# Optimization experiments

Measured on AMD Instinct MI355X. Metric: run time of the kernel, lower is better.

The kernel has to match this reference:

```python
import jax, jax.numpy as jnp
import numpy as np

T = 5          # temporal frames
WS = 8         # window size (square)
HEADS = 6
DIM = 192      # output channels; qkv input channels = 3*DIM
SHIFT = WS // 2
HDIM = DIM // HEADS
SCALE = HDIM ** -0.5
N = T * WS * WS  # tokens per window = 320


def _rel_index():
    # Faithful replication of the torch buffer construction (including the
    # quirk that the dw channel gets no offset).
    coords = np.stack(np.meshgrid(np.arange(T), np.arange(WS), np.arange(WS), indexing='ij'))
    cf = coords.reshape(3, -1)                      # (3, N)
    rel = (cf[:, :, None] - cf[:, None, :]).transpose(1, 2, 0).astype(np.int64)
    rel[:, :, 0] += WS - 1                          # dt channel
    rel[:, :, 1] += WS - 1                          # dh channel
    rel[:, :, 0] *= 2 * WS - 1
    return rel.sum(-1)                               # (N, N) int

REL_INDEX = jnp.asarray(_rel_index())


def setup_inputs() -> dict:
    key = jax.random.key(0)
    k1, k2, k3, k4 = jax.random.split(key, 4)
    B, H, W = 2, 64, 64
    C = 3 * DIM
    qkv = jax.random.normal(k1, (B, T * H * W, C), jnp.float32)
    bias_table = jax.random.normal(k2, ((T * 2 * WS - 1) * (2 * WS - 1), HEADS), jnp.float32) * 0.02
    proj_w = jax.random.normal(k3, (DIM, DIM), jnp.float32) / np.sqrt(DIM)
    proj_b = jax.random.normal(k4, (DIM,), jnp.float32) * 0.01
    # Standard Swin shifted-window attention mask, tiled over T (t-outer order).
    img = np.zeros((H, W), np.float32)
    cnt = 0
    sls = (slice(0, -WS), slice(-WS, -SHIFT), slice(-SHIFT, None))
    for hs in sls:
        for ws_ in sls:
            img[hs, ws_] = cnt
            cnt += 1
    mw = img.reshape(H // WS, WS, W // WS, WS).transpose(0, 2, 1, 3).reshape(-1, WS * WS)
    mw = np.tile(mw, (1, T))                         # (nW, N)
    am = mw[:, None, :] - mw[:, :, None]
    mask = jnp.asarray(np.where(am != 0, -100.0, 0.0).astype(np.float32))
    return {'qkv': qkv, 'bias_table': bias_table, 'proj_w': proj_w,
            'proj_b': proj_b, 'mask': mask, 'H': H, 'W': W}


def reference(qkv, bias_table, proj_w, proj_b, mask, H, W):
    B, L, C = qkv.shape
    x = qkv.reshape(B, T, H, W, C)
    # cyclic shift
    x = jnp.roll(x, shift=(-SHIFT, -SHIFT), axis=(2, 3))
    # window partition -> (B*nW, N, C)
    x = x.reshape(B, T, H // WS, WS, W // WS, WS, C)
    x = x.transpose(0, 2, 4, 1, 3, 5, 6).reshape(-1, N, C)
    B_ = x.shape[0]
    qkv_ = x.reshape(B_, N, 3, HEADS, HDIM).transpose(2, 0, 3, 1, 4)  # (3,B_,h,N,d)
    q, k, v = qkv_[0] * SCALE, qkv_[1], qkv_[2]
    attn = jnp.einsum('bhqd,bhkd->bhqk', q, k)       # (B_, h, N, N)
    rpb = bias_table[REL_INDEX.reshape(-1)].reshape(N, N, HEADS).transpose(2, 0, 1)
    attn = attn + rpb[None]
    nW = mask.shape[0]
    attn = attn.reshape(B_ // nW, nW, HEADS, N, N) + mask[None, :, None]
    attn = jax.nn.softmax(attn.reshape(B_, HEADS, N, N), axis=-1)
    out = jnp.einsum('bhqk,bhkd->bhqd', attn, v)     # (B_, h, N, d)
    out = out.transpose(0, 2, 1, 3).reshape(B_, N, DIM)
    out = out @ proj_w.T + proj_b
    # window reverse -> (B, T, H, W, DIM)
    out = out.reshape(B, H // WS, W // WS, T, WS, WS, DIM)
    out = out.transpose(0, 3, 1, 4, 2, 5, 6).reshape(B, T, H, W, DIM)
    out = jnp.roll(out, shift=(SHIFT, SHIFT), axis=(2, 3))
    return out.reshape(B, T * H * W, DIM)
```

## Files before the change

### kernel.cpp

```cpp
#include <hip/hip_runtime.h>
#include <hip/hip_bf16.h>

#define TT      5
#define NHEADS  6
#define DIMC    192
#define SHIFT_  4
#define HDIM_   32
#define NTOK    320
#define NWIN    64
#define BATCH   2
#define LOG2E   1.44269504088896f
#define SCALE_LOG2E (0.17677669529663687f * 1.44269504088896f)
#define NEGMASK (-100.0f * 1.44269504088896f)

typedef short short8v __attribute__((ext_vector_type(8)));
typedef float floatx4 __attribute__((ext_vector_type(4)));
union FragU { uint4 u; short8v s; };

static __device__ __forceinline__ float bf16lo(unsigned u) {
    union { unsigned i; float f; } x; x.i = u << 16; return x.f;
}
static __device__ __forceinline__ float bf16hi(unsigned u) {
    union { unsigned i; float f; } x; x.i = u & 0xffff0000u; return x.f;
}
static __device__ __forceinline__ unsigned short bf16b(float f) {
    __hip_bfloat16 h = __float2bfloat16(f);
    unsigned short u; __builtin_memcpy(&u, &h, 2); return u;
}
static __device__ __forceinline__ unsigned pk2(float a, float b) {
    return (unsigned)bf16b(a) | ((unsigned)bf16b(b) << 16);
}

static __device__ __forceinline__ bool detect_bf16(const unsigned* q) {
    uint4 w = ((const uint4*)q)[threadIdx.x & 63];
    int cnt = 0;
    unsigned e;
    e = (w.x >> 7) & 0xffu; cnt += (e >= 100u && e <= 135u);
    e = (w.y >> 7) & 0xffu; cnt += (e >= 100u && e <= 135u);
    e = (w.z >> 7) & 0xffu; cnt += (e >= 100u && e <= 135u);
    e = (w.w >> 7) & 0xffu; cnt += (e >= 100u && e <= 135u);
    unsigned long long m = __ballot(cnt >= 2);
    return __popcll(m) >= 32;
}

__global__ __launch_bounds__(NTOK) void attn_mfma(
    const void* __restrict__ qkv_raw,
    const void* __restrict__ bias_raw,
    __hip_bfloat16* __restrict__ win_out)
{
    const bool isbf = detect_bf16((const unsigned*)qkv_raw);
    const int b_  = blockIdx.x;
    const int h   = blockIdx.y;
    const int bb  = b_ >> 6;
    const int wdx = b_ & 63;
    const int wi  = wdx >> 3, wj = wdx & 7;
    const int tid = threadIdx.x;
    const int w    = tid >> 6;
    const int lane = tid & 63;
    const int l15  = lane & 15;
    const int quad = lane >> 4;

    __shared__ unsigned short sK[320 * 40];
    __shared__ unsigned short sVT[32 * 328];
    __shared__ unsigned short sP[5 * 64 * 40];
    __shared__ float sRS[5 * 64];
    __shared__ float sBias[192];

    {
        const int n = tid;
        const int t = n >> 6, s = n & 63, hl = s >> 3, wl = s & 7;
        const int gh = (wi * 8 + hl + SHIFT_) & 63;
        const int gw = (wj * 8 + wl + SHIFT_) & 63;
        const long grow = (long)bb * (TT * 64 * 64) + t * 4096 + gh * 64 + gw;
        if (!isbf) {
            const float* base = (const float*)qkv_raw + grow * (3 * DIMC);
            const float* kp = base + DIMC + h * HDIM_;
            uint4* dst = (uint4*)&sK[n * 40];
            #pragma unroll
            for (int i = 0; i < 4; i++)
                dst[i] = make_uint4(pk2(kp[8*i+0], kp[8*i+1]), pk2(kp[8*i+2], kp[8*i+3]),
                                    pk2(kp[8*i+4], kp[8*i+5]), pk2(kp[8*i+6], kp[8*i+7]));
            const float* vp = base + 2 * DIMC + h * HDIM_;
            #pragma unroll
            for (int d = 0; d < 32; d++) sVT[d * 328 + n] = bf16b(vp[d]);
            for (int i = tid; i < 192; i += NTOK)
                sBias[i] = ((const float*)bias_raw)[i * NHEADS + h] * LOG2E;
        } else {
            const __hip_bfloat16* base = (const __hip_bfloat16*)qkv_raw + grow * (3 * DIMC);
            const uint4* kp = (const uint4*)(base + DIMC + h * HDIM_);
            uint4* dst = (uint4*)&sK[n * 40];
            #pragma unroll
            for (int i = 0; i < 4; i++) dst[i] = kp[i];
            const unsigned* vp = (const unsigned*)(base + 2 * DIMC + h * HDIM_);
            #pragma unroll
            for (int i = 0; i < 16; i++) {
                unsigned u = vp[i];
                sVT[(2*i+0) * 328 + n] = (unsigned short)(u & 0xffffu);
                sVT[(2*i+1) * 328 + n] = (unsigned short)(u >> 16);
            }
            for (int i = tid; i < 192; i += NTOK)
                sBias[i] = __bfloat162float(((const __hip_bfloat16*)bias_raw)[i * NHEADS + h]) * LOG2E;
        }
    }

    FragU qf[4];
    int cn_q[4], labq[4];
    #pragma unroll
    for (int jq = 0; jq < 4; jq++) {
        const int qtok = w * 64 + jq * 16 + l15;
        const int t = qtok >> 6, s = qtok & 63, hl = s >> 3, wl = s & 7;
        cn_q[jq] = t * 15 + hl + wl;
        const int hh = wi * 8 + hl, ww = wj * 8 + wl;
        labq[jq] = ((hh < 56) ? 0 : ((hh < 60) ? 1 : 2)) * 3 +
                   ((ww < 56) ? 0 : ((ww < 60) ? 1 : 2));
        const int gh = (wi * 8 + hl + SHIFT_) & 63;
        const int gw = (wj * 8 + wl + SHIFT_) & 63;
        const long grow = (long)bb * (TT * 64 * 64) + t * 4096 + gh * 64 + gw;
        if (!isbf) {
            const float* qp = (const float*)qkv_raw + grow * (3 * DIMC) + h * HDIM_ + quad * 8;
            qf[jq].u = make_uint4(
                pk2(qp[0]*SCALE_LOG2E, qp[1]*SCALE_LOG2E), pk2(qp[2]*SCALE_LOG2E, qp[3]*SCALE_LOG2E),
                pk2(qp[4]*SCALE_LOG2E, qp[5]*SCALE_LOG2E), pk2(qp[6]*SCALE_LOG2E, qp[7]*SCALE_LOG2E));
        } else {
            const uint4 uu = *(const uint4*)((const __hip_bfloat16*)qkv_raw + grow * (3 * DIMC) + h * HDIM_ + quad * 8);
            qf[jq].u = make_uint4(
                pk2(bf16lo(uu.x)*SCALE_LOG2E, bf16hi(uu.x)*SCALE_LOG2E),
                pk2(bf16lo(uu.y)*SCALE_LOG2E, bf16hi(uu.y)*SCALE_LOG2E),
                pk2(bf16lo(uu.z)*SCALE_LOG2E, bf16hi(uu.z)*SCALE_LOG2E),
                pk2(bf16lo(uu.w)*SCALE_LOG2E, bf16hi(uu.w)*SCALE_LOG2E));
        }
    }
    __syncthreads();

    unsigned short* sPw = &sP[w * 64 * 40];
    const floatx4 z4 = {0.f, 0.f, 0.f, 0.f};
    floatx4 oacc[4][2];
    #pragma unroll
    for (int i = 0; i < 4; i++) { oacc[i][0] = z4; oacc[i][1] = z4; }
    float rs[4] = {0.f, 0.f, 0.f, 0.f};

    for (int kb = 0; kb < 10; kb++) {
        FragU kf[2], vf[2];
        kf[0].u = *(const uint4*)&sK[(kb * 32 + l15) * 40 + quad * 8];
        kf[1].u = *(const uint4*)&sK[(kb * 32 + 16 + l15) * 40 + quad * 8];
        vf[0].u = *(const uint4*)&sVT[l15 * 328 + kb * 32 + quad * 8];
        vf[1].u = *(const uint4*)&sVT[(16 + l15) * 328 + kb * 32 + quad * 8];

        floatx4 sv[2][4];
        #pragma unroll
        for (int kt = 0; kt < 2; kt++)
            #pragma unroll
            for (int jq = 0; jq < 4; jq++)
                sv[kt][jq] = __builtin_amdgcn_mfma_f32_16x16x32_bf16(kf[kt].s, qf[jq].s, z4, 0, 0, 0);

        int cjv[2][4], labk[2][4];
        #pragma unroll
        for (int kt = 0; kt < 2; kt++) {
            const int kbase = kb * 32 + kt * 16;
            const int tk = kbase >> 6;
            const int Ck = (7 - tk) * 15 + 7;
            const int sh = ((kbase & 63) >> 3) + (quad >> 1);
            const int rhk = (wi == 7) ? ((sh < 4) ? 1 : 2) : 0;
            #pragma unroll
            for (int reg = 0; reg < 4; reg++) {
                const int sw = (quad & 1) * 4 + reg;
                cjv[kt][reg] = Ck - sh - sw;
                const int rwk = (wj == 7) ? ((sw < 4) ? 1 : 2) : 0;
                labk[kt][reg] = rhk * 3 + rwk;
            }
        }
        #pragma unroll
        for (int kt = 0; kt < 2; kt++)
            #pragma unroll
            for (int jq = 0; jq < 4; jq++) {
                float e[4];
                #pragma unroll
                for (int reg = 0; reg < 4; reg++) {
                    const float bv = sBias[cn_q[jq] + cjv[kt][reg]];
                    const float mv = (labk[kt][reg] != labq[jq]) ? NEGMASK : 0.f;
                    e[reg] = exp2f(sv[kt][jq][reg] + bv + mv);
                }
                rs[jq] += (e[0] + e[1]) + (e[2] + e[3]);
                *(uint2*)&sPw[(jq * 16 + l15) * 40 + kt * 16 + quad * 4] =
                    make_uint2(pk2(e[0], e[1]), pk2(e[2], e[3]));
            }

        #pragma unroll
        for (int i = 0; i < 4; i++) {
            FragU pf; pf.u = *(const uint4*)&sPw[(i * 16 + l15) * 40 + quad * 8];
            oacc[i][0] = __builtin_amdgcn_mfma_f32_16x16x32_bf16(pf.s, vf[0].s, oacc[i][0], 0, 0, 0);
            oacc[i][1] = __builtin_amdgcn_mfma_f32_16x16x32_bf16(pf.s, vf[1].s, oacc[i][1], 0, 0, 0);
        }
    }

    #pragma unroll
    for (int jq = 0; jq < 4; jq++) {
        float r = rs[jq];
        r += __shfl_xor(r, 16);
        r += __shfl_xor(r, 32);
        if (lane < 16) sRS[w * 64 + jq * 16 + lane] = r;
    }
    #pragma unroll
    for (int i = 0; i < 4; i++) {
        float inv[4];
        #pragma unroll
        for (int reg = 0; reg < 4; reg++)
            inv[reg] = 1.0f / sRS[w * 64 + i * 16 + quad * 4 + reg];
        #pragma unroll
        for (int nt = 0; nt < 2; nt++) {
            #pragma unroll
            for (int reg = 0; reg < 4; reg++) {
                const int q = w * 64 + i * 16 + quad * 4 + reg;
                win_out[((long)b_ * NTOK + q) * DIMC + h * HDIM_ + nt * 16 + l15] =
                    __float2bfloat16(oacc[i][nt][reg] * inv[reg]);
            }
        }
    }
}

__global__ __launch_bounds__(256) void proj_mfma(
    const __hip_bfloat16* __restrict__ win,
    const void* __restrict__ w_raw,
    const void* __restrict__ b_raw,
    const unsigned* __restrict__ sniff,
    void* __restrict__ out_raw)
{
    const bool isbf = detect_bf16(sniff);
    __shared__ unsigned short sW[192 * 200];
    __shared__ float sBp[192];
    const int tid = threadIdx.x;

    if (!isbf) {
        const float2* wsrc = (const float2*)w_raw;
        for (int i = tid; i < 192 * 96; i += 256) {
            int r = i / 96, c2 = i - r * 96;
            float2 ab = wsrc[i];
            *(unsigned*)&sW[r * 200 + c2 * 2] = pk2(ab.x, ab.y);
        }
        for (int i = tid; i < 192; i += 256) sBp[i] = ((const float*)b_raw)[i];
    } else {
        const unsigned* wsrc = (const unsigned*)w_raw;
        for (int i = tid; i < 192 * 96; i += 256) {
            int r = i / 96, c2 = i - r * 96;
            *(unsigned*)&sW[r * 200 + c2 * 2] = wsrc[i];
        }
        for (int i = tid; i < 192; i += 256)
            sBp[i] = __bfloat162float(((const __hip_bfloat16*)b_raw)[i]);
    }
    __syncthreads();

    const int w    = tid >> 6;
    const int lane = tid & 63;
    const int l15  = lane & 15;
    const int quad = lane >> 4;
    const int tok0 = blockIdx.x * 64 + w * 16;

    const floatx4 z4 = {0.f, 0.f, 0.f, 0.f};
    floatx4 acc[12];
    #pragma unroll
    for (int nt = 0; nt < 12; nt++) acc[nt] = z4;

    #pragma unroll
    for (int k0 = 0; k0 < 192; k0 += 32) {
        FragU af;
        af.u = *(const uint4*)(win + ((long)tok0 + l15) * DIMC + k0 + quad * 8);
        #pragma unroll
        for (int nt = 0; nt < 12; nt++) {
            FragU bf_;
            bf_.u = *(const uint4*)&sW[(nt * 16 + l15) * 200 + k0 + quad * 8];
            acc[nt] = __builtin_amdgcn_mfma_f32_16x16x32_bf16(af.s, bf_.s, acc[nt], 0, 0, 0);
        }
    }

    long rowoff[4];
    #pragma unroll
    for (int reg = 0; reg < 4; reg++) {
        const int token = tok0 + quad * 4 + reg;
        const int bw = token / NTOK;
        const int nn = token - bw * NTOK;
        const int bb = bw >> 6, wdx = bw & 63, wi2 = wdx >> 3, wj2 = wdx & 7;
        const int t = nn >> 6, s2 = nn & 63, hl = s2 >> 3, wl = s2 & 7;
        const int gh = (wi2 * 8 + hl + SHIFT_) & 63;
        const int gw = (wj2 * 8 + wl + SHIFT_) & 63;
        rowoff[reg] = ((long)bb * (TT * 64 * 64) + t * 4096 + gh * 64 + gw) * DIMC;
    }
    #pragma unroll
    for (int nt = 0; nt < 12; nt++) {
        const int o = nt * 16 + l15;
        const float bias = sBp[o];
        #pragma unroll
        for (int reg = 0; reg < 4; reg++) {
            const float v = acc[nt][reg] + bias;
            if (!isbf) ((float*)out_raw)[rowoff[reg] + o] = v;
            else       ((__hip_bfloat16*)out_raw)[rowoff[reg] + o] = __float2bfloat16(v);
        }
    }
}

extern "C" void kernel_launch(void* const* d_in, const int* in_sizes, int n_in,
                              void* d_out, int out_size, void* d_ws, size_t ws_size,
                              hipStream_t stream)
{
    (void)in_sizes; (void)n_in; (void)out_size; (void)ws_size;
    const void* qkv        = d_in[0];
    const void* bias_table = d_in[1];
    const void* proj_w     = d_in[2];
    const void* proj_b     = d_in[3];
    __hip_bfloat16* win = (__hip_bfloat16*)d_ws;

    attn_mfma<<<dim3(BATCH * NWIN, NHEADS), NTOK, 0, stream>>>(qkv, bias_table, win);
    proj_mfma<<<dim3(BATCH * NWIN * NTOK / 64), 256, 0, stream>>>(
        (const __hip_bfloat16*)win, proj_w, proj_b, (const unsigned*)qkv, d_out);
}
```

Measured before the change: 245.7 us.

## Stream K from global into registers with prefetch, pre-convert projection weights

The attention kernel stops staging K in shared memory. Each wave now loads its K fragments straight from global memory into registers, prefetching the next 16-token tile while the current one is processed, and asks for higher occupancy through launch bounds. A separate small kernel converts the projection weights and bias to bf16/fp32 once per call, so the projection kernel no longer fills a large shared-memory weight tile in every block. P values are packed with a cheaper round-to-nearest bit trick. The cost is redundant K reads from global memory across waves, an extra kernel launch, and weight reads in the projection kernel that now go to L2 instead of LDS.

Result: slower. 269.5 us (+9.7%).

```diff
diff --git a/kernel.cpp b/kernel.cpp
--- a/kernel.cpp
+++ b/kernel.cpp
@@ -30,6 +30,10 @@
 static __device__ __forceinline__ unsigned pk2(float a, float b) {
     return (unsigned)bf16b(a) | ((unsigned)bf16b(b) << 16);
 }
+static __device__ __forceinline__ unsigned pk2h(float a, float b) {
+    unsigned ua = __float_as_uint(a), ub = __float_as_uint(b);
+    return ((ua + 0x8000u) >> 16) | ((ub + 0x8000u) & 0xffff0000u);
+}
 
 static __device__ __forceinline__ bool detect_bf16(const unsigned* q) {
     uint4 w = ((const uint4*)q)[threadIdx.x & 63];
@@ -43,7 +47,7 @@
     return __popcll(m) >= 32;
 }
 
-__global__ __launch_bounds__(NTOK) void attn_mfma(
+__global__ __launch_bounds__(NTOK, 4) void attn_mfma(
     const void* __restrict__ qkv_raw,
     const void* __restrict__ bias_raw,
     __hip_bfloat16* __restrict__ win_out)
@@ -60,11 +64,10 @@
     const int l15  = lane & 15;
     const int quad = lane >> 4;
 
-    __shared__ unsigned short sK[320 * 40];
     __shared__ unsigned short sVT[32 * 328];
     __shared__ unsigned short sP[5 * 64 * 40];
-    __shared__ float sRS[5 * 64];
     __shared__ float sBias[192];
+    __shared__ float sRS[320];
 
     {
         const int n = tid;
@@ -73,33 +76,21 @@
         const int gw = (wj * 8 + wl + SHIFT_) & 63;
         const long grow = (long)bb * (TT * 64 * 64) + t * 4096 + gh * 64 + gw;
         if (!isbf) {
-            const float* base = (const float*)qkv_raw + grow * (3 * DIMC);
-            const float* kp = base + DIMC + h * HDIM_;
-            uint4* dst = (uint4*)&sK[n * 40];
-            #pragma unroll
-            for (int i = 0; i < 4; i++)
-                dst[i] = make_uint4(pk2(kp[8*i+0], kp[8*i+1]), pk2(kp[8*i+2], kp[8*i+3]),
-                                    pk2(kp[8*i+4], kp[8*i+5]), pk2(kp[8*i+6], kp[8*i+7]));
-            const float* vp = base + 2 * DIMC + h * HDIM_;
+            const float* vp = (const float*)qkv_raw + grow * (3 * DIMC) + 2 * DIMC + h * HDIM_;
             #pragma unroll
             for (int d = 0; d < 32; d++) sVT[d * 328 + n] = bf16b(vp[d]);
-            for (int i = tid; i < 192; i += NTOK)
-                sBias[i] = ((const float*)bias_raw)[i * NHEADS + h] * LOG2E;
+            if (tid < 192)
+                sBias[tid] = ((const float*)bias_raw)[tid * NHEADS + h] * LOG2E;
         } else {
-            const __hip_bfloat16* base = (const __hip_bfloat16*)qkv_raw + grow * (3 * DIMC);
-            const uint4* kp = (const uint4*)(base + DIMC + h * HDIM_);
-            uint4* dst = (uint4*)&sK[n * 40];
-            #pragma unroll
-            for (int i = 0; i < 4; i++) dst[i] = kp[i];
-            const unsigned* vp = (const unsigned*)(base + 2 * DIMC + h * HDIM_);
+            const unsigned* vp = (const unsigned*)((const __hip_bfloat16*)qkv_raw + grow * (3 * DIMC) + 2 * DIMC + h * HDIM_);
             #pragma unroll
             for (int i = 0; i < 16; i++) {
                 unsigned u = vp[i];
                 sVT[(2*i+0) * 328 + n] = (unsigned short)(u & 0xffffu);
                 sVT[(2*i+1) * 328 + n] = (unsigned short)(u >> 16);
             }
-            for (int i = tid; i < 192; i += NTOK)
-                sBias[i] = __bfloat162float(((const __hip_bfloat16*)bias_raw)[i * NHEADS + h]) * LOG2E;
+            if (tid < 192)
+                sBias[tid] = __bfloat162float(((const __hip_bfloat16*)bias_raw)[tid * NHEADS + h]) * LOG2E;
         }
     }
 
@@ -130,6 +121,36 @@
                 pk2(bf16lo(uu.w)*SCALE_LOG2E, bf16hi(uu.w)*SCALE_LOG2E));
         }
     }
+
+    auto koff = [&](int m16) -> long {
+        const int token = m16 * 16 + l15;
+        const int t = token >> 6, s = token & 63, hl2 = s >> 3, wl2 = s & 7;
+        const int gh2 = (wi * 8 + hl2 + SHIFT_) & 63;
+        const int gw2 = (wj * 8 + wl2 + SHIFT_) & 63;
+        return ((long)bb * (TT * 64 * 64) + t * 4096 + gh2 * 64 + gw2) * (3 * DIMC)
+               + DIMC + h * HDIM_ + quad * 8;
+    };
+    auto loadKt = [&](uint4* d, int m16) {
+        const long off = koff(m16);
+        if (!isbf) {
+            const uint4* p = (const uint4*)((const float*)qkv_raw + off);
+            d[0] = p[0]; d[1] = p[1];
+        } else {
+            d[0] = *(const uint4*)((const __hip_bfloat16*)qkv_raw + off);
+        }
+    };
+    auto cvtKt = [&](const uint4* d) -> FragU {
+        FragU kf;
+        if (!isbf) {
+            const float* f = (const float*)d;
+            kf.u = make_uint4(pk2(f[0], f[1]), pk2(f[2], f[3]),
+                              pk2(f[4], f[5]), pk2(f[6], f[7]));
+        } else kf.u = d[0];
+        return kf;
+    };
+
+    uint4 rA[2], rB[2];
+    loadKt(rA, 0);
     __syncthreads();
 
     unsigned short* sPw = &sP[w * 64 * 40];
@@ -139,57 +160,50 @@
     for (int i = 0; i < 4; i++) { oacc[i][0] = z4; oacc[i][1] = z4; }
     float rs[4] = {0.f, 0.f, 0.f, 0.f};
 
-    for (int kb = 0; kb < 10; kb++) {
-        FragU kf[2], vf[2];
-        kf[0].u = *(const uint4*)&sK[(kb * 32 + l15) * 40 + quad * 8];
-        kf[1].u = *(const uint4*)&sK[(kb * 32 + 16 + l15) * 40 + quad * 8];
-        vf[0].u = *(const uint4*)&sVT[l15 * 328 + kb * 32 + quad * 8];
-        vf[1].u = *(const uint4*)&sVT[(16 + l15) * 328 + kb * 32 + quad * 8];
-
-        floatx4 sv[2][4];
-        #pragma unroll
-        for (int kt = 0; kt < 2; kt++)
-            #pragma unroll
-            for (int jq = 0; jq < 4; jq++)
-                sv[kt][jq] = __builtin_amdgcn_mfma_f32_16x16x32_bf16(kf[kt].s, qf[jq].s, z4, 0, 0, 0);
-
-        int cjv[2][4], labk[2][4];
-        #pragma unroll
-        for (int kt = 0; kt < 2; kt++) {
-            const int kbase = kb * 32 + kt * 16;
-            const int tk = kbase >> 6;
-            const int Ck = (7 - tk) * 15 + 7;
-            const int sh = ((kbase & 63) >> 3) + (quad >> 1);
-            const int rhk = (wi == 7) ? ((sh < 4) ? 1 : 2) : 0;
+    auto do_kt = [&](int kb, int kt, const FragU& kf) {
+        floatx4 sv[4];
+        #pragma unroll
+        for (int jq = 0; jq < 4; jq++)
+            sv[jq] = __builtin_amdgcn_mfma_f32_16x16x32_bf16(kf.s, qf[jq].s, z4, 0, 0, 0);
+        const int kbase = kb * 32 + kt * 16;
+        const int Ck = (7 - (kbase >> 6)) * 15 + 7;
+        const int sh = ((kbase & 63) >> 3) + (quad >> 1);
+        const int rhk = (wi == 7) ? ((sh < 4) ? 1 : 2) : 0;
+        int cjv[4], labk[4];
+        #pragma unroll
+        for (int reg = 0; reg < 4; reg++) {
+            const int sw = (quad & 1) * 4 + reg;
+            cjv[reg] = Ck - sh - sw;
+            labk[reg] = rhk * 3 + ((wj == 7) ? ((sw < 4) ? 1 : 2) : 0);
+        }
+        #pragma unroll
+        for (int jq = 0; jq < 4; jq++) {
+            float e[4];
             #pragma unroll
             for (int reg = 0; reg < 4; reg++) {
-                const int sw = (quad & 1) * 4 + reg;
-                cjv[kt][reg] = Ck - sh - sw;
-                const int rwk = (wj == 7) ? ((sw < 4) ? 1 : 2) : 0;
-                labk[kt][reg] = rhk * 3 + rwk;
+                const float bv = sBias[cn_q[jq] + cjv[reg]];
+                const float mv = (labk[reg] != labq[jq]) ? NEGMASK : 0.f;
+                e[reg] = exp2f(sv[jq][reg] + bv + mv);
             }
-        }
-        #pragma unroll
-        for (int kt = 0; kt < 2; kt++)
-            #pragma unroll
-            for (int jq = 0; jq < 4; jq++) {
-                float e[4];
-                #pragma unroll
-                for (int reg = 0; reg < 4; reg++) {
-                    const float bv = sBias[cn_q[jq] + cjv[kt][reg]];
-                    const float mv = (labk[kt][reg] != labq[jq]) ? NEGMASK : 0.f;
-                    e[reg] = exp2f(sv[kt][jq][reg] + bv + mv);
-                }
-                rs[jq] += (e[0] + e[1]) + (e[2] + e[3]);
-                *(uint2*)&sPw[(jq * 16 + l15) * 40 + kt * 16 + quad * 4] =
-                    make_uint2(pk2(e[0], e[1]), pk2(e[2], e[3]));
-            }
-
+            rs[jq] += (e[0] + e[1]) + (e[2] + e[3]);
+            *(uint2*)&sPw[(jq * 16 + l15) * 40 + kt * 16 + quad * 4] =
+                make_uint2(pk2h(e[0], e[1]), pk2h(e[2], e[3]));
+        }
+    };
+
+    for (int kb = 0; kb < 10; kb++) {
+        loadKt(rB, 2 * kb + 1);
+        { FragU kf = cvtKt(rA); do_kt(kb, 0, kf); }
+        if (kb < 9) loadKt(rA, 2 * kb + 2);
+        FragU vf0, vf1;
+        vf0.u = *(const uint4*)&sVT[l15 * 328 + kb * 32 + quad * 8];
+        vf1.u = *(const uint4*)&sVT[(16 + l15) * 328 + kb * 32 + quad * 8];
+        { FragU kf = cvtKt(rB); do_kt(kb, 1, kf); }
         #pragma unroll
         for (int i = 0; i < 4; i++) {
             FragU pf; pf.u = *(const uint4*)&sPw[(i * 16 + l15) * 40 + quad * 8];
-            oacc[i][0] = __builtin_amdgcn_mfma_f32_16x16x32_bf16(pf.s, vf[0].s, oacc[i][0], 0, 0, 0);
-            oacc[i][1] = __builtin_amdgcn_mfma_f32_16x16x32_bf16(pf.s, vf[1].s, oacc[i][1], 0, 0, 0);
+            oacc[i][0] = __builtin_amdgcn_mfma_f32_16x16x32_bf16(pf.s, vf0.s, oacc[i][0], 0, 0, 0);
+            oacc[i][1] = __builtin_amdgcn_mfma_f32_16x16x32_bf16(pf.s, vf1.s, oacc[i][1], 0, 0, 0);
         }
     }
 
@@ -218,37 +232,31 @@
     }
 }
 
+__global__ __launch_bounds__(256) void prep_w(
+    const void* __restrict__ w_raw, const void* __restrict__ b_raw,
+    const unsigned* __restrict__ sniff,
+    unsigned short* __restrict__ wbf, float* __restrict__ bf32)
+{
+    const bool isbf = detect_bf16(sniff);
+    const int g = blockIdx.x * 256 + threadIdx.x;
+    if (!isbf) wbf[g] = bf16b(((const float*)w_raw)[g]);
+    else       wbf[g] = ((const unsigned short*)w_raw)[g];
+    if (blockIdx.x == 0 && threadIdx.x < 192) {
+        bf32[threadIdx.x] = isbf
+            ? __bfloat162float(((const __hip_bfloat16*)b_raw)[threadIdx.x])
+            : ((const float*)b_raw)[threadIdx.x];
+    }
+}
+
 __global__ __launch_bounds__(256) void proj_mfma(
     const __hip_bfloat16* __restrict__ win,
-    const void* __restrict__ w_raw,
-    const void* __restrict__ b_raw,
+    const unsigned short* __restrict__ wbf,
+    const float* __restrict__ bf32,
     const unsigned* __restrict__ sniff,
     void* __restrict__ out_raw)
 {
     const bool isbf = detect_bf16(sniff);
-    __shared__ unsigned short sW[192 * 200];
-    __shared__ float sBp[192];
-    const int tid = threadIdx.x;
-
-    if (!isbf) {
-        const float2* wsrc = (const float2*)w_raw;
-        for (int i = tid; i < 192 * 96; i += 256) {
-            int r = i / 96, c2 = i - r * 96;
-            float2 ab = wsrc[i];
-            *(unsigned*)&sW[r * 200 + c2 * 2] = pk2(ab.x, ab.y);
-        }
-        for (int i = tid; i < 192; i += 256) sBp[i] = ((const float*)b_raw)[i];
-    } else {
-        const unsigned* wsrc = (const unsigned*)w_raw;
-        for (int i = tid; i < 192 * 96; i += 256) {
-            int r = i / 96, c2 = i - r * 96;
-            *(unsigned*)&sW[r * 200 + c2 * 2] = wsrc[i];
-        }
-        for (int i = tid; i < 192; i += 256)
-            sBp[i] = __bfloat162float(((const __hip_bfloat16*)b_raw)[i]);
-    }
-    __syncthreads();
-
+    const int tid  = threadIdx.x;
     const int w    = tid >> 6;
     const int lane = tid & 63;
     const int l15  = lane & 15;
@@ -261,13 +269,13 @@
     for (int nt = 0; nt < 12; nt++) acc[nt] = z4;
 
     #pragma unroll
-    for (int k0 = 0; k0 < 192; k0 += 32) {
+    for (int ks = 0; ks < 6; ks++) {
         FragU af;
-        af.u = *(const uint4*)(win + ((long)tok0 + l15) * DIMC + k0 + quad * 8);
+        af.u = *(const uint4*)(win + ((long)tok0 + l15) * DIMC + ks * 32 + quad * 8);
         #pragma unroll
         for (int nt = 0; nt < 12; nt++) {
             FragU bf_;
-            bf_.u = *(const uint4*)&sW[(nt * 16 + l15) * 200 + k0 + quad * 8];
+            bf_.u = *(const uint4*)(wbf + (nt * 16 + l15) * DIMC + ks * 32 + quad * 8);
             acc[nt] = __builtin_amdgcn_mfma_f32_16x16x32_bf16(af.s, bf_.s, acc[nt], 0, 0, 0);
         }
     }
@@ -287,7 +295,7 @@
     #pragma unroll
     for (int nt = 0; nt < 12; nt++) {
         const int o = nt * 16 + l15;
-        const float bias = sBp[o];
+        const float bias = bf32[o];
         #pragma unroll
         for (int reg = 0; reg < 4; reg++) {
             const float v = acc[nt][reg] + bias;
@@ -306,9 +314,13 @@
     const void* bias_table = d_in[1];
     const void* proj_w     = d_in[2];
     const void* proj_b     = d_in[3];
+
     __hip_bfloat16* win = (__hip_bfloat16*)d_ws;
-
+    unsigned short* wbf = (unsigned short*)((char*)d_ws + 15728640);
+    float*          bfb = (float*)((char*)d_ws + 15802368);
+
+    prep_w<<<dim3(144), 256, 0, stream>>>(proj_w, proj_b, (const unsigned*)qkv, wbf, bfb);
     attn_mfma<<<dim3(BATCH * NWIN, NHEADS), NTOK, 0, stream>>>(qkv, bias_table, win);
     proj_mfma<<<dim3(BATCH * NWIN * NTOK / 64), 256, 0, stream>>>(
-        (const __hip_bfloat16*)win, proj_w, proj_b, (const unsigned*)qkv, d_out);
-}
+        win, wbf, bfb, (const unsigned*)qkv, d_out);
+}
```
